# Kernel optimization log

Hardware: AMD Instinct MI355X
Metric: run time of the kernel (lower is better)

The kernel has to match this reference:

```python
import jax, jax.numpy as jnp
import numpy as np

B, N, D, H = 1, 4096, 1024, 16
K = D // H
ROPE_BASE = 10000.0


def _rope_cos_sin(n, k, base, dtype):
    # GPT-NeoX style rotary embedding: inv_freq over even dims, emb = cat(freqs, freqs)
    inv_freq = 1.0 / (base ** (jnp.arange(0, k, 2, dtype=jnp.float32) / k))  # [K/2]
    pos = jnp.arange(n, dtype=jnp.float32)
    freqs = pos[:, None] * inv_freq[None, :]              # [N, K/2]
    emb = jnp.concatenate([freqs, freqs], axis=-1)        # [N, K]
    return jnp.cos(emb).astype(dtype), jnp.sin(emb).astype(dtype)


def _rotate_half(x):
    x1, x2 = jnp.split(x, 2, axis=-1)
    return jnp.concatenate([-x2, x1], axis=-1)


def setup_inputs() -> dict:
    key = jax.random.key(0)
    kx, kq, ko = jax.random.split(key, 3)
    x = jax.random.normal(kx, (B, N, D), dtype=jnp.float32)
    # torch Linear weights: [out_features, in_features], y = x @ W^T
    w_qkv = jax.random.normal(kq, (3 * H * K, D), dtype=jnp.float32) / np.sqrt(D)
    w_out = jax.random.normal(ko, (D, D), dtype=jnp.float32) / np.sqrt(D)
    return {"x": x, "w_qkv": w_qkv, "w_out": w_out}


def reference(x, w_qkv, w_out):
    b, n, d = x.shape
    qkv = jnp.einsum('bnd,ed->bne', x, w_qkv).reshape(b, n, 3, H, K)
    q, k, v = qkv[:, :, 0], qkv[:, :, 1], qkv[:, :, 2]   # [B, N, H, K]
    cos, sin = _rope_cos_sin(n, K, ROPE_BASE, x.dtype)    # [N, K]
    cos = cos[None, :, None, :]
    sin = sin[None, :, None, :]
    q = q * cos + _rotate_half(q) * sin
    k = k * cos + _rotate_half(k) * sin
    # explicit O(N^2) score matrix, as in the original module
    scores = jnp.einsum('bnhk,bmhk->bnhm', q, k) / np.sqrt(K).astype(x.dtype)
    causal_mask = jnp.tril(jnp.ones((n, n), dtype=bool))  # [N, M]
    scores = jnp.where(causal_mask[None, :, None, :], scores, jnp.finfo(x.dtype).min)
    probs = jax.nn.softmax(scores, axis=-1)
    attn = jnp.einsum('bnhm,bmhk->bnhk', probs, v).reshape(b, n, d)
    return jnp.einsum('bnd,ed->bne', attn, w_out)
```

## Files before the change

kernel.cpp:

```cpp
#include <hip/hip_runtime.h>
#include <hip/hip_bf16.h>
#include <math.h>

#define N_SEQ 4096
#define DIM   1024
#define NHEAD 16
#define HDIM  64
#define E3    3072

typedef short bf16x8 __attribute__((ext_vector_type(8)));
typedef float f32x4  __attribute__((ext_vector_type(4)));
typedef unsigned int u32;

__device__ __forceinline__ float bf2f(unsigned short u) {
    union { unsigned int i; float f; } x; x.i = ((unsigned int)u) << 16; return x.f;
}
__device__ __forceinline__ unsigned short f2bf(float f) {
    union { float f; unsigned int i; } x; x.f = f;
    unsigned int r = x.i + 0x7FFF + ((x.i >> 16) & 1);
    return (unsigned short)(r >> 16);
}
__device__ __forceinline__ unsigned short f2bf_fast(float f) {
    union { float f; unsigned int i; } x; x.f = f;
    return (unsigned short)((x.i + 0x8000u) >> 16);
}
__device__ __forceinline__ f32x4 mfma16(bf16x8 a, bf16x8 b, f32x4 c) {
    return __builtin_amdgcn_mfma_f32_16x16x32_bf16(a, b, c, 0, 0, 0);
}
__device__ __forceinline__ void gload_lds16(const unsigned short* g, unsigned short* l) {
    __builtin_amdgcn_global_load_lds(
        (const __attribute__((address_space(1))) u32*)g,
        (__attribute__((address_space(3))) u32*)l, 16, 0, 0);
}

__global__ void detect_dtype_kernel(const unsigned short* __restrict__ X, int* __restrict__ flag) {
    __shared__ int cnt;
    if (threadIdx.x == 0) cnt = 0;
    __syncthreads();
    int bad = 0;
    for (int i = threadIdx.x; i < 4096; i += 256) {
        float v = bf2f(X[i]);
        if (!(fabsf(v) < 1e10f)) bad = 1;
    }
    if (bad) atomicAdd(&cnt, 1);
    __syncthreads();
    if (threadIdx.x == 0) *flag = (cnt > 0) ? 1 : 0;
}

__global__ __launch_bounds__(256)
void convert_kernel(const void* __restrict__ src, unsigned short* __restrict__ dst,
                    int n4, const int* __restrict__ flag)
{
    const int isf32 = *flag;
    const int stride = gridDim.x * blockDim.x;
    for (int i = blockIdx.x * blockDim.x + threadIdx.x; i < n4; i += stride) {
        if (isf32) {
            float4 v = ((const float4*)src)[i];
            ushort4 u;
            u.x = f2bf(v.x); u.y = f2bf(v.y); u.z = f2bf(v.z); u.w = f2bf(v.w);
            ((ushort4*)dst)[i] = u;
        } else {
            ((ushort4*)dst)[i] = ((const ushort4*)src)[i];
        }
    }
}

__global__ __launch_bounds__(256)
void qkv_mfma_kernel(const unsigned short* __restrict__ Xb,
                     const unsigned short* __restrict__ Wb,
                     unsigned short* __restrict__ Qf,
                     unsigned short* __restrict__ Kf,
                     unsigned short* __restrict__ Vf)
{
    __shared__ unsigned short As[128 * 32];
    __shared__ unsigned short Bs[128 * 32];

    const int tid  = threadIdx.x;
    const int lane = tid & 63;
    const int wave = tid >> 6;
    const int wr = wave >> 1, wc = wave & 1;
    const int lm = lane & 15, q4 = lane >> 4;
    const int rbase = blockIdx.y * 128;
    const int cbase = blockIdx.x * 128;

    const int srow = wave * 16 + (lane >> 2);
    const int scol = (lane & 3) * 8;

    f32x4 acc[4][4];
    #pragma unroll
    for (int i = 0; i < 4; ++i)
        #pragma unroll
        for (int j = 0; j < 4; ++j) acc[i][j] = (f32x4){0.f, 0.f, 0.f, 0.f};

    for (int kt = 0; kt < DIM; kt += 32) {
        #pragma unroll
        for (int j = 0; j < 2; ++j) {
            gload_lds16(Xb + (size_t)(rbase + j*64 + srow) * DIM + kt + scol,
                        &As[j*2048 + wave*512]);
            gload_lds16(Wb + (size_t)(cbase + j*64 + srow) * DIM + kt + scol,
                        &Bs[j*2048 + wave*512]);
        }
        __syncthreads();

        bf16x8 a[4], b[4];
        #pragma unroll
        for (int mi = 0; mi < 4; ++mi)
            a[mi] = *(const bf16x8*)&As[(wr*64 + mi*16 + lm)*32 + q4*8];
        #pragma unroll
        for (int ni = 0; ni < 4; ++ni)
            b[ni] = *(const bf16x8*)&Bs[(wc*64 + ni*16 + lm)*32 + q4*8];
        #pragma unroll
        for (int mi = 0; mi < 4; ++mi)
            #pragma unroll
            for (int ni = 0; ni < 4; ++ni)
                acc[mi][ni] = mfma16(a[mi], b[ni], acc[mi][ni]);

        __syncthreads();
    }

    const int ecol = cbase + wc * 64;
    const int part = ecol >> 10;
    const int h    = (ecol >> 6) & 15;

    if (part == 2) {
        #pragma unroll
        for (int mi = 0; mi < 4; ++mi)
            #pragma unroll
            for (int r = 0; r < 4; ++r) {
                const int n = rbase + wr*64 + mi*16 + q4*4 + r;
                #pragma unroll
                for (int ni = 0; ni < 4; ++ni) {
                    size_t idx = ((((size_t)h*128 + (n >> 5))*4 + ni) << 9)
                               + ((size_t)(lm | (((n >> 3) & 3) << 4)) << 3) + (n & 7);
                    Vf[idx] = f2bf(acc[mi][ni][r]);
                }
            }
    } else {
        unsigned short* dst = (part == 0) ? Qf : Kf;
        const float scl = (part == 0) ? 0.180336884f : 1.0f;
        const float inv0 = powf(10000.f, -((float)lm)        * (1.f/32.f));
        const float inv1 = powf(10000.f, -((float)(lm + 16)) * (1.f/32.f));
        #pragma unroll
        for (int mi = 0; mi < 4; ++mi)
            #pragma unroll
            for (int r = 0; r < 4; ++r) {
                const int n = rbase + wr*64 + mi*16 + q4*4 + r;
                const size_t tb = ((size_t)(h*256 + (n >> 4))) << 10;
                #pragma unroll
                for (int ni = 0; ni < 2; ++ni) {
                    const int d = ni*16 + lm;
                    float s, c;
                    sincosf((float)n * (ni ? inv1 : inv0), &s, &c);
                    const float vlo = (acc[mi][ni][r]*c - acc[mi][ni+2][r]*s) * scl;
                    const float vhi = (acc[mi][ni+2][r]*c + acc[mi][ni][r]*s) * scl;
                    const size_t idx = tb + ((size_t)((n & 15) | (((d >> 3) & 3) << 4)) << 3) + (d & 7);
                    dst[idx]       = f2bf(vlo);
                    dst[idx + 512] = f2bf(vhi);
                }
            }
    }
}

__global__ __launch_bounds__(256)
void attn_mfma_kernel(const unsigned short* __restrict__ Qf,
                      const unsigned short* __restrict__ Kf,
                      const unsigned short* __restrict__ Vf,
                      unsigned short* __restrict__ Attn)
{
    __shared__ __align__(16) unsigned short Ks[2][4096];
    __shared__ __align__(16) unsigned short Vs[2][4096];
    __shared__ __align__(16) unsigned short P16[4][16][72];

    const int tid  = threadIdx.x;
    const int lane = tid & 63;
    const int wave = tid >> 6;
    const int q4 = lane >> 4, lm = lane & 15;

    const int h  = blockIdx.x & 15;
    const int qb = blockIdx.x >> 4;
    const int q0 = (63 - qb) << 6;
    const int qw = q0 + (wave << 4);

    const size_t qbase = (((size_t)(h*256 + (qw >> 4))) << 10) + (size_t)lane * 8;
    const bf16x8 aq0 = *(const bf16x8*)(Qf + qbase);
    const bf16x8 aq1 = *(const bf16x8*)(Qf + qbase + 512);

    float l_part[4];
    f32x4 o[4];
    #pragma unroll
    for (int r = 0; r < 4; ++r) l_part[r] = 0.f;
    #pragma unroll
    for (int dc = 0; dc < 4; ++dc) o[dc] = (f32x4){0.f, 0.f, 0.f, 0.f};

    unsigned short* pw = &P16[wave][0][0];
    const int ntiles = (q0 >> 6) + 1;

    #define STAGE(buf, kt_)                                                        \
        {                                                                          \
            const size_t ktile = ((size_t)(h*256 + ((kt_) >> 4))) << 10;           \
            const size_t vtile = ((size_t)(h*128 + ((kt_) >> 5))) << 11;           \
            if (wave < 2) {                                                        \
                _Pragma("unroll")                                                  \
                for (int i = 0; i < 4; ++i) {                                      \
                    const int ch = wave*4 + i;                                     \
                    gload_lds16(Kf + ktile + ch*512 + lane*8, &Ks[buf][ch*512]);   \
                }                                                                  \
            } else {                                                               \
                _Pragma("unroll")                                                  \
                for (int i = 0; i < 4; ++i) {                                      \
                    const int ch = (wave - 2)*4 + i;                               \
                    gload_lds16(Vf + vtile + ch*512 + lane*8, &Vs[buf][ch*512]);   \
                }                                                                  \
            }                                                                      \
        }

    STAGE(0, 0)

    for (int it = 0; it < ntiles; ++it) {
        const int kt = it << 6;
        const int cur = it & 1;

        __syncthreads();
        if (it + 1 < ntiles) STAGE(cur ^ 1, kt + 64)

        f32x4 s[4];
        #pragma unroll
        for (int t = 0; t < 4; ++t) {
            const bf16x8 bk0 = *(const bf16x8*)&Ks[cur][t*1024 + lane*8];
            const bf16x8 bk1 = *(const bf16x8*)&Ks[cur][t*1024 + 512 + lane*8];
            f32x4 z = (f32x4){0.f, 0.f, 0.f, 0.f};
            z = mfma16(aq0, bk0, z);
            s[t] = mfma16(aq1, bk1, z);
        }

        if (kt + 63 > qw) {
            #pragma unroll
            for (int t = 0; t < 4; ++t) {
                const int key = kt + 16*t + lm;
                #pragma unroll
                for (int r = 0; r < 4; ++r)
                    if (key > qw + 4*q4 + r) s[t][r] = -INFINITY;
            }
        }

        #pragma unroll
        for (int t = 0; t < 4; ++t)
            #pragma unroll
            for (int r = 0; r < 4; ++r) {
                const float p = exp2f(s[t][r]);
                l_part[r] += p;
                pw[(4*q4 + r)*72 + 16*t + lm] = f2bf_fast(p);
            }

        const bf16x8 pa0 = *(const bf16x8*)(pw + lm*72 + 8*q4);
        const bf16x8 pa1 = *(const bf16x8*)(pw + lm*72 + 32 + 8*q4);

        #pragma unroll
        for (int dc = 0; dc < 4; ++dc) {
            const bf16x8 bv0 = *(const bf16x8*)&Vs[cur][dc*512 + lane*8];
            const bf16x8 bv1 = *(const bf16x8*)&Vs[cur][2048 + dc*512 + lane*8];
            o[dc] = mfma16(pa0, bv0, o[dc]);
            o[dc] = mfma16(pa1, bv1, o[dc]);
        }
    }
    #undef STAGE

    float inv[4];
    #pragma unroll
    for (int r = 0; r < 4; ++r) {
        float l = l_part[r];
        #pragma unroll
        for (int mk = 1; mk <= 8; mk <<= 1) l += __shfl_xor(l, mk);
        inv[r] = 1.f / l;
    }
    #pragma unroll
    for (int dc = 0; dc < 4; ++dc)
        #pragma unroll
        for (int r = 0; r < 4; ++r)
            Attn[(size_t)(qw + 4*q4 + r) * DIM + (h << 6) + 16*dc + lm] = f2bf(o[dc][r] * inv[r]);
}

__global__ __launch_bounds__(256)
void out_mfma_kernel(const unsigned short* __restrict__ Ab,
                     const unsigned short* __restrict__ Wb,
                     const int* __restrict__ flag,
                     void* __restrict__ Out)
{
    __shared__ unsigned short As[128 * 32];
    __shared__ unsigned short Bs[64 * 32];

    const int isf32 = *flag;
    const int tid  = threadIdx.x;
    const int lane = tid & 63;
    const int wave = tid >> 6;
    const int lm = lane & 15, q4 = lane >> 4;
    const int rbase = blockIdx.y * 128;
    const int cbase = blockIdx.x * 64;

    const int srow16 = lane >> 2;
    const int scol = (lane & 3) * 8;

    f32x4 acc[2][4];
    #pragma unroll
    for (int i = 0; i < 2; ++i)
        #pragma unroll
        for (int j = 0; j < 4; ++j) acc[i][j] = (f32x4){0.f, 0.f, 0.f, 0.f};

    for (int kt = 0; kt < DIM; kt += 32) {
        #pragma unroll
        for (int j = 0; j < 2; ++j) {
            const int row = wave*32 + j*16 + srow16;
            gload_lds16(Ab + (size_t)(rbase + row) * DIM + kt + scol,
                        &As[(wave*32 + j*16)*32]);
        }
        {
            const int row = wave*16 + srow16;
            gload_lds16(Wb + (size_t)(cbase + row) * DIM + kt + scol,
                        &Bs[(wave*16)*32]);
        }
        __syncthreads();

        bf16x8 a[2], b[4];
        #pragma unroll
        for (int mi = 0; mi < 2; ++mi)
            a[mi] = *(const bf16x8*)&As[(wave*32 + mi*16 + lm)*32 + q4*8];
        #pragma unroll
        for (int ni = 0; ni < 4; ++ni)
            b[ni] = *(const bf16x8*)&Bs[(ni*16 + lm)*32 + q4*8];
        #pragma unroll
        for (int mi = 0; mi < 2; ++mi)
            #pragma unroll
            for (int ni = 0; ni < 4; ++ni)
                acc[mi][ni] = mfma16(a[mi], b[ni], acc[mi][ni]);

        __syncthreads();
    }

    #pragma unroll
    for (int mi = 0; mi < 2; ++mi)
        #pragma unroll
        for (int r = 0; r < 4; ++r) {
            const size_t n = rbase + wave*32 + mi*16 + q4*4 + r;
            #pragma unroll
            for (int ni = 0; ni < 4; ++ni) {
                const size_t e = cbase + ni*16 + lm;
                const float v = acc[mi][ni][r];
                if (isf32) ((float*)Out)[n * DIM + e] = v;
                else       ((unsigned short*)Out)[n * DIM + e] = f2bf(v);
            }
        }
}

extern "C" void kernel_launch(void* const* d_in, const int* in_sizes, int n_in,
                              void* d_out, int out_size, void* d_ws, size_t ws_size,
                              hipStream_t stream) {
    const void* X    = d_in[0];
    const void* Wqkv = d_in[1];
    const void* Wout = d_in[2];

    int* flag = (int*)d_ws;
    unsigned short* base = (unsigned short*)((char*)d_ws + 256);
    const size_t nX = (size_t)N_SEQ * DIM;
    const size_t nWq = (size_t)E3 * DIM;
    const size_t nWo = (size_t)DIM * DIM;
    unsigned short* Xb  = base;
    unsigned short* Wqb = Xb + nX;
    unsigned short* Wob = Wqb + nWq;
    unsigned short* Qf  = Wob + nWo;
    unsigned short* Kf  = Qf + nX;
    unsigned short* Vf  = Kf + nX;
    unsigned short* At  = Vf + nX;

    detect_dtype_kernel<<<1, 256, 0, stream>>>((const unsigned short*)X, flag);
    convert_kernel<<<512, 256, 0, stream>>>(X,    Xb,  (int)(nX  >> 2), flag);
    convert_kernel<<<512, 256, 0, stream>>>(Wqkv, Wqb, (int)(nWq >> 2), flag);
    convert_kernel<<<256, 256, 0, stream>>>(Wout, Wob, (int)(nWo >> 2), flag);

    qkv_mfma_kernel<<<dim3(E3 / 128, N_SEQ / 128), 256, 0, stream>>>(Xb, Wqb, Qf, Kf, Vf);
    attn_mfma_kernel<<<dim3(NHEAD * (N_SEQ / 64)), 256, 0, stream>>>(Qf, Kf, Vf, At);
    out_mfma_kernel<<<dim3(DIM / 64, N_SEQ / 128), 256, 0, stream>>>(At, Wob, flag, d_out);
}
```

Measured before the change: 236.8 us.

## Fuse dtype probe and conversions into one prep kernel; serpentine attention block order

Replaces the separate dtype-detect kernel and three conversion launches with a single prep kernel in which every block probes the input dtype and converts X and both weights in one grid-stride loop. The bf16 path now skips the copy, with the GEMM kernels choosing original or converted buffers from the flag. The attention grid is also remapped from longest-causal-first to a serpentine ordering of query blocks within groups of 16. Every prep block repeats the probe, and the new ordering may change load balance across CUs.

```diff
diff --git a/kernel.cpp b/kernel.cpp
--- a/kernel.cpp
+++ b/kernel.cpp
@@ -33,7 +33,7 @@
         (__attribute__((address_space(3))) u32*)l, 16, 0, 0);
 }
 
-__global__ void detect_dtype_kernel(const unsigned short* __restrict__ X, int* __restrict__ flag) {
+__device__ __forceinline__ int probe_isf32(const unsigned short* __restrict__ X) {
     __shared__ int cnt;
     if (threadIdx.x == 0) cnt = 0;
     __syncthreads();
@@ -44,36 +44,51 @@
     }
     if (bad) atomicAdd(&cnt, 1);
     __syncthreads();
-    if (threadIdx.x == 0) *flag = (cnt > 0) ? 1 : 0;
+    return cnt > 0;
 }
 
 __global__ __launch_bounds__(256)
-void convert_kernel(const void* __restrict__ src, unsigned short* __restrict__ dst,
-                    int n4, const int* __restrict__ flag)
+void prep_kernel(const void* __restrict__ X, const void* __restrict__ Wq,
+                 const void* __restrict__ Wo,
+                 unsigned short* __restrict__ Xb, unsigned short* __restrict__ Wqb,
+                 unsigned short* __restrict__ Wob,
+                 int* __restrict__ flag)
 {
-    const int isf32 = *flag;
+    const int isf32 = probe_isf32((const unsigned short*)X);
+    if (blockIdx.x == 0 && threadIdx.x == 0) *flag = isf32;
+    if (!isf32) return;
+
+    const int nX4  = (N_SEQ * DIM) >> 2;
+    const int nWq4 = (E3 * DIM) >> 2;
+    const int nWo4 = (DIM * DIM) >> 2;
+    const int total = nX4 + nWq4 + nWo4;
     const int stride = gridDim.x * blockDim.x;
-    for (int i = blockIdx.x * blockDim.x + threadIdx.x; i < n4; i += stride) {
-        if (isf32) {
-            float4 v = ((const float4*)src)[i];
-            ushort4 u;
-            u.x = f2bf(v.x); u.y = f2bf(v.y); u.z = f2bf(v.z); u.w = f2bf(v.w);
-            ((ushort4*)dst)[i] = u;
-        } else {
-            ((ushort4*)dst)[i] = ((const ushort4*)src)[i];
-        }
+    for (int i = blockIdx.x * blockDim.x + threadIdx.x; i < total; i += stride) {
+        const float4* src; ushort4* dst; int j = i;
+        if (j < nX4)            { src = (const float4*)X  + j;  dst = (ushort4*)Xb  + j; }
+        else if ((j -= nX4) < nWq4) { src = (const float4*)Wq + j;  dst = (ushort4*)Wqb + j; }
+        else { j -= nWq4;         src = (const float4*)Wo + j;  dst = (ushort4*)Wob + j; }
+        float4 v = *src;
+        ushort4 u;
+        u.x = f2bf(v.x); u.y = f2bf(v.y); u.z = f2bf(v.z); u.w = f2bf(v.w);
+        *dst = u;
     }
 }
 
 __global__ __launch_bounds__(256)
-void qkv_mfma_kernel(const unsigned short* __restrict__ Xb,
-                     const unsigned short* __restrict__ Wb,
+void qkv_mfma_kernel(const void* __restrict__ Xo, const unsigned short* __restrict__ Xc,
+                     const void* __restrict__ Wo_, const unsigned short* __restrict__ Wc,
+                     const int* __restrict__ flag,
                      unsigned short* __restrict__ Qf,
                      unsigned short* __restrict__ Kf,
                      unsigned short* __restrict__ Vf)
 {
     __shared__ unsigned short As[128 * 32];
     __shared__ unsigned short Bs[128 * 32];
+
+    const int isf32 = *flag;
+    const unsigned short* Xb = isf32 ? Xc : (const unsigned short*)Xo;
+    const unsigned short* Wb = isf32 ? Wc : (const unsigned short*)Wo_;
 
     const int tid  = threadIdx.x;
     const int lane = tid & 63;
@@ -176,10 +191,13 @@
     const int wave = tid >> 6;
     const int q4 = lane >> 4, lm = lane & 15;
 
-    const int h  = blockIdx.x & 15;
-    const int qb = blockIdx.x >> 4;
-    const int q0 = (63 - qb) << 6;
-    const int qw = q0 + (wave << 4);
+    const int h    = blockIdx.x & 15;
+    const int w    = blockIdx.x >> 4;
+    const int draw = w >> 4;
+    const int qi   = w & 15;
+    const int qb   = (draw << 4) | ((draw & 1) ? (15 - qi) : qi);
+    const int q0   = qb << 6;
+    const int qw   = q0 + (wave << 4);
 
     const size_t qbase = (((size_t)(h*256 + (qw >> 4))) << 10) + (size_t)lane * 8;
     const bf16x8 aq0 = *(const bf16x8*)(Qf + qbase);
@@ -282,7 +300,7 @@
 
 __global__ __launch_bounds__(256)
 void out_mfma_kernel(const unsigned short* __restrict__ Ab,
-                     const unsigned short* __restrict__ Wb,
+                     const void* __restrict__ Wo_, const unsigned short* __restrict__ Wc,
                      const int* __restrict__ flag,
                      void* __restrict__ Out)
 {
@@ -290,6 +308,8 @@
     __shared__ unsigned short Bs[64 * 32];
 
     const int isf32 = *flag;
+    const unsigned short* Wb = isf32 ? Wc : (const unsigned short*)Wo_;
+
     const int tid  = threadIdx.x;
     const int lane = tid & 63;
     const int wave = tid >> 6;
@@ -371,12 +391,8 @@
     unsigned short* Vf  = Kf + nX;
     unsigned short* At  = Vf + nX;
 
-    detect_dtype_kernel<<<1, 256, 0, stream>>>((const unsigned short*)X, flag);
-    convert_kernel<<<512, 256, 0, stream>>>(X,    Xb,  (int)(nX  >> 2), flag);
-    convert_kernel<<<512, 256, 0, stream>>>(Wqkv, Wqb, (int)(nWq >> 2), flag);
-    convert_kernel<<<256, 256, 0, stream>>>(Wout, Wob, (int)(nWo >> 2), flag);
-
-    qkv_mfma_kernel<<<dim3(E3 / 128, N_SEQ / 128), 256, 0, stream>>>(Xb, Wqb, Qf, Kf, Vf);
+    prep_kernel<<<768, 256, 0, stream>>>(X, Wqkv, Wout, Xb, Wqb, Wob, flag);
+    qkv_mfma_kernel<<<dim3(E3 / 128, N_SEQ / 128), 256, 0, stream>>>(X, Xb, Wqkv, Wqb, flag, Qf, Kf, Vf);
     attn_mfma_kernel<<<dim3(NHEAD * (N_SEQ / 64)), 256, 0, stream>>>(Qf, Kf, Vf, At);
-    out_mfma_kernel<<<dim3(DIM / 64, N_SEQ / 128), 256, 0, stream>>>(At, Wob, flag, d_out);
-}
+    out_mfma_kernel<<<dim3(DIM / 64, N_SEQ / 128), 256, 0, stream>>>(At, Wout, Wob, flag, d_out);
+}
```

Measured after the change: 243.3 us. +2.7%, slower.
